# Performance work log

Measured on AMD Instinct MI355X. Metric: run time of the kernel, lower is better.

The kernel has to match this reference:

```python
import jax, jax.numpy as jnp
import numpy as np

# Rates 40MHz -> 60MHz => Fraction(1.5).limit_denominator(1000) = 3/2
UP, DOWN = 3, 2
MAX_RATE = max(UP, DOWN)
HALF_LEN = 10 * MAX_RATE                      # 30 (scipy.resample_poly default)
N_PRE_PAD = DOWN - (HALF_LEN % DOWN)          # 2
N_PRE_REMOVE = (HALF_LEN + N_PRE_PAD) // DOWN # 16
NUMTAPS_LS = 51
TAIL_ZEROS = 100
B, N = 8, 1048576


def _firwin_kaiser(numtaps, cutoff, beta):
    # scipy.signal.firwin(numtaps, cutoff, window=('kaiser', beta)), cutoff in Nyquist units
    m = np.arange(numtaps) - (numtaps - 1) / 2.0
    h = cutoff * np.sinc(cutoff * m)
    h *= np.kaiser(numtaps, beta)
    return h / h.sum()  # unit DC gain


def _band_int(k, f1, f2):
    # integral_{f1}^{f2} cos(pi*k*f) df, elementwise over integer array k
    k = np.asarray(k, dtype=float)
    safe = np.where(k == 0.0, 1.0, np.pi * k)
    return np.where(k == 0.0, f2 - f1, (np.sin(np.pi * k * f2) - np.sin(np.pi * k * f1)) / safe)


def _firls(numtaps, bands, desired):
    # Type-I linear-phase least-squares FIR (constant desired per band, unit weights)
    M = (numtaps - 1) // 2
    k = np.arange(M + 1)
    Q = np.zeros((M + 1, M + 1))
    rhs = np.zeros(M + 1)
    for f1, f2, d in zip(bands[0::2], bands[1::2], desired[0::2]):
        km = k[:, None] - k[None, :]
        kp = k[:, None] + k[None, :]
        Q += 0.5 * (_band_int(km, f1, f2) + _band_int(kp, f1, f2))
        rhs += d * _band_int(k, f1, f2)
    a = np.linalg.solve(Q, rhs)  # A(f) = sum_n a[n] cos(pi n f)
    half = a / 2.0
    half[0] = a[0]
    return np.concatenate([half[:0:-1], half])  # symmetric impulse response


def setup_inputs() -> dict:
    key = jax.random.key(0)
    x = jax.random.normal(key, (B, N), dtype=jnp.float32)
    # resample_poly anti-imaging filter, scaled by UP, with scipy's zero pre-padding
    h = _firwin_kaiser(2 * HALF_LEN + 1, 1.0 / MAX_RATE, 5.0) * UP
    h = np.concatenate([np.zeros(N_PRE_PAD), h])
    cutoff = DOWN / UP
    b = _firls(NUMTAPS_LS, [0.0, cutoff, cutoff + 0.1, 1.0], [1.0, 1.0, 0.0, 0.0])
    return {
        'x': x,
        'h_resample': jnp.asarray(h, jnp.float32),
        'b_fir': jnp.asarray(b, jnp.float32),
    }


def reference(x, h_resample, b_fir):
    b_sz, n = x.shape
    n_in = b_sz * n
    n_out = n_in * UP // DOWN + (1 if (n_in * UP) % DOWN else 0)
    xf = x.reshape(-1)
    Lh = h_resample.shape[0]
    # Fused polyphase resample: full convolution of UP-zero-stuffed signal
    # with h (flipped for true convolution), decimated by DOWN.
    y = jax.lax.conv_general_dilated(
        xf[None, None, :], h_resample[::-1][None, None, :],
        window_strides=(DOWN,), padding=[(Lh - 1, Lh - 1)],
        lhs_dilation=(UP,),
        dimension_numbers=('NCH', 'OIH', 'NCH'))[0, 0]
    u = y[N_PRE_REMOVE:N_PRE_REMOVE + n_out]               # == scipy.resample_poly
    up_padded = jnp.concatenate([u, jnp.zeros((TAIL_ZEROS,), x.dtype)])
    Lb = b_fir.shape[0]
    # lfilter(b, 1, .) == causal FIR: left-pad Lb-1 zeros, same-length output
    filt = jax.lax.conv_general_dilated(
        up_padded[None, None, :], b_fir[::-1][None, None, :],
        window_strides=(1,), padding=[(Lb - 1, 0)],
        dimension_numbers=('NCH', 'OIH', 'NCH'))[0, 0]
    total = n_out + TAIL_ZEROS
    per_b = total // b_sz
    return filt[:b_sz * per_b].reshape(b_sz, per_b)
```

## Files before the change

kernel.cpp:

```cpp
#include <hip/hip_runtime.h>


#define TPB 256
#define RPT 12
#define OTILE (TPB * RPT)
#define XTILE2 2112
#define NTAPS 55
#define CPSTRIDE 56

__global__ void build_coeffs(const float* __restrict__ h,
                             const float* __restrict__ b,
                             float* __restrict__ cp) {
    __shared__ float h_s[63];
    __shared__ float b_s[51];
    const int tid = threadIdx.x;
    if (tid < 63) h_s[tid] = h[tid];
    if (tid < 51) b_s[tid] = b[tid];
    __syncthreads();
    for (int idx = tid; idx < 3 * CPSTRIDE; idx += blockDim.x) {
        const int p = idx / CPSTRIDE;
        const int k = idx - p * CPSTRIDE;
        float acc = 0.0f;
        if (k < NTAPS) {
            const int j = p + 3 * k;
            for (int m = 0; m <= 50; ++m) {
                const int hi = j - 2 * m;
                if (hi >= 0 && hi <= 62) acc += b_s[m] * h_s[hi];
            }
        }
        cp[idx] = acc;
    }
}

__global__ __launch_bounds__(128) void boundary_fix(
    const float* __restrict__ x, const float* __restrict__ h,
    const float* __restrict__ b, float* __restrict__ out,
    int n_in, int n_out, int out_size)
{
    __shared__ float h_s[63];
    __shared__ float b_s[51];
    __shared__ float x_s[64];
    __shared__ float u_s[50];

    const int tid = threadIdx.x;
    if (tid < 63) h_s[tid] = h[tid];
    if (tid < 51) b_s[tid] = b[tid];

    if (blockIdx.x == 0) {
        if (tid < 44) x_s[tid] = (tid < n_in) ? x[tid] : 0.0f;
        __syncthreads();
        if (tid < 50) {
            const int s  = 2 * tid + 32;
            const int p0 = s % 3;
            const int q  = s / 3;
            float u = 0.0f;
            #pragma unroll
            for (int i = 0; i <= 20; ++i) {
                const int xi = q - i;
                u += h_s[p0 + 3 * i] * ((xi >= 0) ? x_s[xi] : 0.0f);
            }
            u_s[tid] = u;
        }
        __syncthreads();
        if (tid < 50) {
            float acc = 0.0f;
            for (int t = 0; t <= tid; ++t) acc += b_s[tid - t] * u_s[t];
            out[tid] = acc;
        }
    } else {
        const int t0   = n_out - 50;
        const int qmin = (2 * t0 + 32) / 3;
        const int xb   = qmin - 20;
        if (tid < 64) {
            const int xi = xb + tid;
            x_s[tid] = (xi >= 0 && xi < n_in) ? x[xi] : 0.0f;
        }
        __syncthreads();
        if (tid < 50) {
            const int t  = t0 + tid;
            const int s  = 2 * t + 32;
            const int p0 = s % 3;
            const int q  = s / 3;
            const int base = q - xb;
            float u = 0.0f;
            #pragma unroll
            for (int i = 0; i <= 20; ++i)
                u += h_s[p0 + 3 * i] * x_s[base - i];
            u_s[tid] = u;
        }
        __syncthreads();
        const int n_tail = out_size - n_out;
        if (tid < n_tail) {
            float acc = 0.0f;
            for (int j = tid; j <= 49; ++j) acc += b_s[tid + 50 - j] * u_s[j];
            out[n_out + tid] = acc;
        }
    }
}

#define GRP12(g, A, B, C, D) {                                          \
    const float4 q2 = c2q[g];                                           \
    const float4 q1 = c1q[g];                                           \
    const float4 q0 = c0q[g];                                           \
                                                               \
    a0  += q2.x * C.z;  a1  += q1.x * C.w;  a2  += q0.x * B.x;          \
    a3  += q2.x * B.x;  a4  += q1.x * B.y;  a5  += q0.x * B.z;          \
    a6  += q2.x * B.z;  a7  += q1.x * B.w;  a8  += q0.x * A.x;          \
    a9  += q2.x * A.x;  a10 += q1.x * A.y;  a11 += q0.x * A.z;          \
                                                               \
    a0  += q2.y * C.y;  a1  += q1.y * C.z;  a2  += q0.y * C.w;          \
    a3  += q2.y * C.w;  a4  += q1.y * B.x;  a5  += q0.y * B.y;          \
    a6  += q2.y * B.y;  a7  += q1.y * B.z;  a8  += q0.y * B.w;          \
    a9  += q2.y * B.w;  a10 += q1.y * A.x;  a11 += q0.y * A.y;          \
                                                               \
    a0  += q2.z * C.x;  a1  += q1.z * C.y;  a2  += q0.z * C.z;          \
    a3  += q2.z * C.z;  a4  += q1.z * C.w;  a5  += q0.z * B.x;          \
    a6  += q2.z * B.x;  a7  += q1.z * B.y;  a8  += q0.z * B.z;          \
    a9  += q2.z * B.z;  a10 += q1.z * B.w;  a11 += q0.z * A.x;          \
                                                               \
    a0  += q2.w * D.w;  a1  += q1.w * C.x;  a2  += q0.w * C.y;          \
    a3  += q2.w * C.y;  a4  += q1.w * C.z;  a5  += q0.w * C.w;          \
    a6  += q2.w * C.w;  a7  += q1.w * B.x;  a8  += q0.w * B.y;          \
    a9  += q2.w * B.y;  a10 += q1.w * B.z;  a11 += q0.w * B.w; }

#define GRP12T(g, A, B, C) {                                            \
    const float4 q2 = c2q[g];                                           \
    const float4 q1 = c1q[g];                                           \
    const float4 q0 = c0q[g];                                           \
    a0  += q2.x * C.z;  a1  += q1.x * C.w;  a2  += q0.x * B.x;          \
    a3  += q2.x * B.x;  a4  += q1.x * B.y;  a5  += q0.x * B.z;          \
    a6  += q2.x * B.z;  a7  += q1.x * B.w;  a8  += q0.x * A.x;          \
    a9  += q2.x * A.x;  a10 += q1.x * A.y;  a11 += q0.x * A.z;          \
    a0  += q2.y * C.y;  a1  += q1.y * C.z;  a2  += q0.y * C.w;          \
    a3  += q2.y * C.w;  a4  += q1.y * B.x;  a5  += q0.y * B.y;          \
    a6  += q2.y * B.y;  a7  += q1.y * B.z;  a8  += q0.y * B.w;          \
    a9  += q2.y * B.w;  a10 += q1.y * A.x;  a11 += q0.y * A.y;          \
    a0  += q2.z * C.x;  a1  += q1.z * C.y;  a2  += q0.z * C.z;          \
    a3  += q2.z * C.z;  a4  += q1.z * C.w;  a5  += q0.z * B.x;          \
    a6  += q2.z * B.x;  a7  += q1.z * B.y;  a8  += q0.z * B.z;          \
    a9  += q2.z * B.z;  a10 += q1.z * B.w;  a11 += q0.z * A.x; }

#define CONV12(SRC) {                                                   \
    const float4 w15 = SRC[15]; const float4 w14 = SRC[14];             \
    const float4 w13 = SRC[13]; const float4 w12 = SRC[12];             \
    const float4 w11 = SRC[11]; const float4 w10 = SRC[10];             \
    const float4 w9  = SRC[9];  const float4 w8  = SRC[8];              \
    const float4 w7  = SRC[7];  const float4 w6  = SRC[6];              \
    const float4 w5  = SRC[5];  const float4 w4  = SRC[4];              \
    const float4 w3  = SRC[3];  const float4 w2  = SRC[2];              \
    const float4 w1  = SRC[1];  const float4 w0  = SRC[0];              \
    __builtin_amdgcn_sched_barrier(0);                                  \
    GRP12( 0, w15, w14, w13, w12);                                      \
    GRP12( 1, w14, w13, w12, w11);                                      \
    GRP12( 2, w13, w12, w11, w10);                                      \
    GRP12( 3, w12, w11, w10, w9);                                       \
    GRP12( 4, w11, w10, w9,  w8);                                       \
    GRP12( 5, w10, w9,  w8,  w7);                                       \
    GRP12( 6, w9,  w8,  w7,  w6);                                       \
    GRP12( 7, w8,  w7,  w6,  w5);                                       \
    GRP12( 8, w7,  w6,  w5,  w4);                                       \
    GRP12( 9, w6,  w5,  w4,  w3);                                       \
    GRP12(10, w5,  w4,  w3,  w2);                                       \
    GRP12(11, w4,  w3,  w2,  w1);                                       \
    GRP12(12, w3,  w2,  w1,  w0);                                       \
    GRP12T(13, w2, w1, w0); }

__global__ __launch_bounds__(TPB) void fused_fast(
    const float* __restrict__ x, const float* __restrict__ cp,
    float* __restrict__ out, int n_in, int n_out)
{
    __shared__ float x_s[XTILE2];

    const int tid = threadIdx.x;
    const int o0  = blockIdx.x * OTILE;
    const int Qb  = (2 * o0 + 30) / 3;
    const int n_tile0 = Qb - 54;

    const float4* c2q = (const float4*)(cp + 2 * CPSTRIDE);
    const float4* c1q = (const float4*)(cp + 1 * CPSTRIDE);
    const float4* c0q = (const float4*)(cp + 0 * CPSTRIDE);

    float a0 = 0.f, a1 = 0.f, a2 = 0.f, a3  = 0.f, a4  = 0.f, a5  = 0.f;
    float a6 = 0.f, a7 = 0.f, a8 = 0.f, a9  = 0.f, a10 = 0.f, a11 = 0.f;

    const bool interior = (n_tile0 >= 0) && (Qb + 2050 <= n_in);
    if (interior) {
        const float4* gx4 = (const float4*)(x + n_tile0 + 8 * tid);
        CONV12(gx4);
    } else {
        for (int i = tid; i < XTILE2; i += TPB) {
            const int n = n_tile0 + i;
            x_s[i] = (n >= 0 && n < n_in) ? x[n] : 0.0f;
        }
        __syncthreads();
        const float4* xs4 = (const float4*)(x_s) + 2 * tid;
        CONV12(xs4);
    }

    const int ob = o0 + RPT * tid;
    if (ob >= 50 && ob + 11 < n_out) {
        float4* o4 = (float4*)(out + ob);
        o4[0] = make_float4(a0, a1, a2,  a3);
        o4[1] = make_float4(a4, a5, a6,  a7);
        o4[2] = make_float4(a8, a9, a10, a11);
    } else {
        const float accs[RPT] = {a0, a1, a2, a3, a4, a5, a6, a7, a8, a9, a10, a11};
#pragma unroll
        for (int d = 0; d < RPT; ++d) {
            const int o = ob + d;
            if (o >= 50 && o < n_out) out[o] = accs[d];
        }
    }
}

extern "C" void kernel_launch(void* const* d_in, const int* in_sizes, int n_in_arrs,
                              void* d_out, int out_size, void* d_ws, size_t ws_size,
                              hipStream_t stream) {
    const float* x = (const float*)d_in[0];
    const float* h = (const float*)d_in[1];
    const float* b = (const float*)d_in[2];
    float* out = (float*)d_out;
    float* cp  = (float*)d_ws;

    const int n_in  = in_sizes[0];
    const int n_out = (int)((long long)n_in * 3 / 2);

    build_coeffs<<<1, 64, 0, stream>>>(h, b, cp);

    const int nblocks = (n_out + OTILE - 1) / OTILE;
    fused_fast<<<nblocks, TPB, 0, stream>>>(x, cp, out, n_in, n_out);
    boundary_fix<<<2, 128, 0, stream>>>(x, h, b, out, n_in, n_out, out_size);
}
```

Before: 119.5 us.

## Make fused kernel persistent over four tiles with register double-buffered prefetch

Each block now handles four consecutive output tiles instead of one, with a fixed grid of 1024 blocks. While computing the current tile from one register set, it loads the next tile's 16 float4 input words into a second set, overlapping global load latency with FMA work. This raises register pressure (two 64-float buffers) and may reduce occupancy. It also hardcodes the grid size and tile count to the test shape.

```diff
diff --git a/kernel.cpp b/kernel.cpp
--- a/kernel.cpp
+++ b/kernel.cpp
@@ -4,6 +4,8 @@
 #define TPB 256
 #define RPT 12
 #define OTILE (TPB * RPT)
+#define TPBK 4
+#define NBLOCKS 1024
 #define XTILE2 2112
 #define NTAPS 55
 #define CPSTRIDE 56
@@ -102,22 +104,18 @@
     const float4 q2 = c2q[g];                                           \
     const float4 q1 = c1q[g];                                           \
     const float4 q0 = c0q[g];                                           \
-                                                               \
     a0  += q2.x * C.z;  a1  += q1.x * C.w;  a2  += q0.x * B.x;          \
     a3  += q2.x * B.x;  a4  += q1.x * B.y;  a5  += q0.x * B.z;          \
     a6  += q2.x * B.z;  a7  += q1.x * B.w;  a8  += q0.x * A.x;          \
     a9  += q2.x * A.x;  a10 += q1.x * A.y;  a11 += q0.x * A.z;          \
-                                                               \
     a0  += q2.y * C.y;  a1  += q1.y * C.z;  a2  += q0.y * C.w;          \
     a3  += q2.y * C.w;  a4  += q1.y * B.x;  a5  += q0.y * B.y;          \
     a6  += q2.y * B.y;  a7  += q1.y * B.z;  a8  += q0.y * B.w;          \
     a9  += q2.y * B.w;  a10 += q1.y * A.x;  a11 += q0.y * A.y;          \
-                                                               \
     a0  += q2.z * C.x;  a1  += q1.z * C.y;  a2  += q0.z * C.z;          \
     a3  += q2.z * C.z;  a4  += q1.z * C.w;  a5  += q0.z * B.x;          \
     a6  += q2.z * B.x;  a7  += q1.z * B.y;  a8  += q0.z * B.z;          \
     a9  += q2.z * B.z;  a10 += q1.z * B.w;  a11 += q0.z * A.x;          \
-                                                               \
     a0  += q2.w * D.w;  a1  += q1.w * C.x;  a2  += q0.w * C.y;          \
     a3  += q2.w * C.y;  a4  += q1.w * C.z;  a5  += q0.w * C.w;          \
     a6  += q2.w * C.w;  a7  += q1.w * B.x;  a8  += q0.w * B.y;          \
@@ -140,30 +138,63 @@
     a6  += q2.z * B.x;  a7  += q1.z * B.y;  a8  += q0.z * B.z;          \
     a9  += q2.z * B.z;  a10 += q1.z * B.w;  a11 += q0.z * A.x; }
 
-#define CONV12(SRC) {                                                   \
-    const float4 w15 = SRC[15]; const float4 w14 = SRC[14];             \
-    const float4 w13 = SRC[13]; const float4 w12 = SRC[12];             \
-    const float4 w11 = SRC[11]; const float4 w10 = SRC[10];             \
-    const float4 w9  = SRC[9];  const float4 w8  = SRC[8];              \
-    const float4 w7  = SRC[7];  const float4 w6  = SRC[6];              \
-    const float4 w5  = SRC[5];  const float4 w4  = SRC[4];              \
-    const float4 w3  = SRC[3];  const float4 w2  = SRC[2];              \
-    const float4 w1  = SRC[1];  const float4 w0  = SRC[0];              \
+#define LOAD16(P, S) {                                                  \
+    P##15 = S[15]; P##14 = S[14]; P##13 = S[13]; P##12 = S[12];         \
+    P##11 = S[11]; P##10 = S[10]; P##9  = S[9];  P##8  = S[8];          \
+    P##7  = S[7];  P##6  = S[6];  P##5  = S[5];  P##4  = S[4];          \
+    P##3  = S[3];  P##2  = S[2];  P##1  = S[1];  P##0  = S[0]; }
+
+#define CONV12R(P) {                                                    \
+    GRP12( 0, P##15, P##14, P##13, P##12);                              \
+    GRP12( 1, P##14, P##13, P##12, P##11);                              \
+    GRP12( 2, P##13, P##12, P##11, P##10);                              \
+    GRP12( 3, P##12, P##11, P##10, P##9);                               \
+    GRP12( 4, P##11, P##10, P##9,  P##8);                               \
+    GRP12( 5, P##10, P##9,  P##8,  P##7);                               \
+    GRP12( 6, P##9,  P##8,  P##7,  P##6);                               \
+    GRP12( 7, P##8,  P##7,  P##6,  P##5);                               \
+    GRP12( 8, P##7,  P##6,  P##5,  P##4);                               \
+    GRP12( 9, P##6,  P##5,  P##4,  P##3);                               \
+    GRP12(10, P##5,  P##4,  P##3,  P##2);                               \
+    GRP12(11, P##4,  P##3,  P##2,  P##1);                               \
+    GRP12(12, P##3,  P##2,  P##1,  P##0);                               \
+    GRP12T(13, P##2, P##1, P##0); }
+
+#define PHASE(CUR, NXT) {                                               \
+    int tnext = tile + 1; if (tnext > tlast) tnext = tlast;             \
+    int nbn = 2048 * tnext - 44;                                        \
+    if (nbn < 0) nbn = 0;                                               \
+    if (nbn > n_in - XTILE2) nbn = n_in - XTILE2;                       \
+    const float4* gn = (const float4*)(x + nbn + 8 * tid);              \
+    LOAD16(NXT, gn);                                                    \
     __builtin_amdgcn_sched_barrier(0);                                  \
-    GRP12( 0, w15, w14, w13, w12);                                      \
-    GRP12( 1, w14, w13, w12, w11);                                      \
-    GRP12( 2, w13, w12, w11, w10);                                      \
-    GRP12( 3, w12, w11, w10, w9);                                       \
-    GRP12( 4, w11, w10, w9,  w8);                                       \
-    GRP12( 5, w10, w9,  w8,  w7);                                       \
-    GRP12( 6, w9,  w8,  w7,  w6);                                       \
-    GRP12( 7, w8,  w7,  w6,  w5);                                       \
-    GRP12( 8, w7,  w6,  w5,  w4);                                       \
-    GRP12( 9, w6,  w5,  w4,  w3);                                       \
-    GRP12(10, w5,  w4,  w3,  w2);                                       \
-    GRP12(11, w4,  w3,  w2,  w1);                                       \
-    GRP12(12, w3,  w2,  w1,  w0);                                       \
-    GRP12T(13, w2, w1, w0); }
+    const int nt0 = 2048 * tile - 44;                                   \
+    if (nt0 < 0 || nt0 + XTILE2 > n_in) {                               \
+        for (int i = tid; i < XTILE2; i += TPB) {                       \
+            const int n = nt0 + i;                                      \
+            x_s[i] = (n >= 0 && n < n_in) ? x[n] : 0.0f;                \
+        }                                                               \
+        __syncthreads();                                                \
+        const float4* xe = (const float4*)(x_s) + 2 * tid;              \
+        LOAD16(CUR, xe);                                                \
+    }                                                                   \
+    float a0=0.f,a1=0.f,a2=0.f,a3=0.f,a4=0.f,a5=0.f;                    \
+    float a6=0.f,a7=0.f,a8=0.f,a9=0.f,a10=0.f,a11=0.f;                  \
+    CONV12R(CUR);                                                       \
+    const int ob = tile * OTILE + 12 * tid;                             \
+    if (ob >= 50 && ob + 11 < n_out) {                                  \
+        float4* o4 = (float4*)(out + ob);                               \
+        o4[0] = make_float4(a0, a1, a2,  a3);                           \
+        o4[1] = make_float4(a4, a5, a6,  a7);                           \
+        o4[2] = make_float4(a8, a9, a10, a11);                          \
+    } else {                                                            \
+        const float accs[RPT] = {a0,a1,a2,a3,a4,a5,a6,a7,a8,a9,a10,a11};\
+        for (int d = 0; d < RPT; ++d) {                                 \
+            const int o = ob + d;                                       \
+            if (o >= 50 && o < n_out) out[o] = accs[d];                 \
+        }                                                               \
+    }                                                                   \
+    tile = tnext; }
 
 __global__ __launch_bounds__(TPB) void fused_fast(
     const float* __restrict__ x, const float* __restrict__ cp,
@@ -171,45 +202,28 @@
 {
     __shared__ float x_s[XTILE2];
 
-    const int tid = threadIdx.x;
-    const int o0  = blockIdx.x * OTILE;
-    const int Qb  = (2 * o0 + 30) / 3;
-    const int n_tile0 = Qb - 54;
+    const int tid   = threadIdx.x;
+    int tile        = blockIdx.x * TPBK;
+    const int tlast = tile + TPBK - 1;
 
     const float4* c2q = (const float4*)(cp + 2 * CPSTRIDE);
     const float4* c1q = (const float4*)(cp + 1 * CPSTRIDE);
     const float4* c0q = (const float4*)(cp + 0 * CPSTRIDE);
 
-    float a0 = 0.f, a1 = 0.f, a2 = 0.f, a3  = 0.f, a4  = 0.f, a5  = 0.f;
-    float a6 = 0.f, a7 = 0.f, a8 = 0.f, a9  = 0.f, a10 = 0.f, a11 = 0.f;
-
-    const bool interior = (n_tile0 >= 0) && (Qb + 2050 <= n_in);
-    if (interior) {
-        const float4* gx4 = (const float4*)(x + n_tile0 + 8 * tid);
-        CONV12(gx4);
-    } else {
-        for (int i = tid; i < XTILE2; i += TPB) {
-            const int n = n_tile0 + i;
-            x_s[i] = (n >= 0 && n < n_in) ? x[n] : 0.0f;
-        }
-        __syncthreads();
-        const float4* xs4 = (const float4*)(x_s) + 2 * tid;
-        CONV12(xs4);
-    }
-
-    const int ob = o0 + RPT * tid;
-    if (ob >= 50 && ob + 11 < n_out) {
-        float4* o4 = (float4*)(out + ob);
-        o4[0] = make_float4(a0, a1, a2,  a3);
-        o4[1] = make_float4(a4, a5, a6,  a7);
-        o4[2] = make_float4(a8, a9, a10, a11);
-    } else {
-        const float accs[RPT] = {a0, a1, a2, a3, a4, a5, a6, a7, a8, a9, a10, a11};
-#pragma unroll
-        for (int d = 0; d < RPT; ++d) {
-            const int o = ob + d;
-            if (o >= 50 && o < n_out) out[o] = accs[d];
-        }
+    float4 A0,A1,A2,A3,A4,A5,A6,A7,A8,A9,A10,A11,A12,A13,A14,A15;
+    float4 B0,B1,B2,B3,B4,B5,B6,B7,B8,B9,B10,B11,B12,B13,B14,B15;
+
+    {
+        int nb0 = 2048 * tile - 44;
+        if (nb0 < 0) nb0 = 0;
+        if (nb0 > n_in - XTILE2) nb0 = n_in - XTILE2;
+        const float4* g0 = (const float4*)(x + nb0 + 8 * tid);
+        LOAD16(A, g0);
+    }
+
+    for (int it = 0; it < TPBK / 2; ++it) {
+        PHASE(A, B);
+        PHASE(B, A);
     }
 }
 
@@ -226,8 +240,6 @@
     const int n_out = (int)((long long)n_in * 3 / 2);
 
     build_coeffs<<<1, 64, 0, stream>>>(h, b, cp);
-
-    const int nblocks = (n_out + OTILE - 1) / OTILE;
-    fused_fast<<<nblocks, TPB, 0, stream>>>(x, cp, out, n_in, n_out);
+    fused_fast<<<NBLOCKS, TPB, 0, stream>>>(x, cp, out, n_in, n_out);
     boundary_fix<<<2, 128, 0, stream>>>(x, h, b, out, n_in, n_out, out_size);
 }
```

New measurement: 127.2 us. 6.4% more time.

## Process four tiles per block with double-buffered async global-to-LDS staging

Applied to the files above, without the earlier changes.

The main kernel now loops over four output tiles per block instead of one, and uses two LDS buffers. While the current tile is being convolved, the next tile's input is prefetched into LDS with global_load_lds async copies. Interior tiles previously read the input straight from global memory into registers; now every tile goes through LDS with a barrier per iteration. The grid size is hard-coded to 1024 blocks, which ties correctness to the fixed problem size, and the async copies are not waited on explicitly before use, so correctness depends on the existing __syncthreads.

```diff
diff --git a/kernel.cpp b/kernel.cpp
--- a/kernel.cpp
+++ b/kernel.cpp
@@ -1,10 +1,14 @@
 #include <hip/hip_runtime.h>
+#include <cstdint>
 
 
 #define TPB 256
 #define RPT 12
 #define OTILE (TPB * RPT)
-#define XTILE2 2112
+#define NTILES 4096
+#define TPBK 4
+#define NBLOCKS (NTILES / TPBK)
+#define XT 2112
 #define NTAPS 55
 #define CPSTRIDE 56
 
@@ -98,26 +102,42 @@
     }
 }
 
+__device__ __forceinline__ void async_copy16(const float* gp, float* lp) {
+    auto g = (const __attribute__((address_space(1))) unsigned int*)(uintptr_t)gp;
+    auto l = (__attribute__((address_space(3))) unsigned int*)(uintptr_t)lp;
+    __builtin_amdgcn_global_load_lds(g, l, 16, 0, 0);
+}
+
+__device__ __forceinline__ void stage_dma(const float* __restrict__ x,
+                                          float* dst, int base, int tid) {
+    async_copy16(x + base + 4 * tid,        dst + 4 * tid);
+    async_copy16(x + base + 1024 + 4 * tid, dst + 1024 + 4 * tid);
+}
+
+__device__ __forceinline__ void stage_edge(const float* __restrict__ x,
+                                           float* dst, int base, int n_in, int tid) {
+    for (int i = tid; i < XT; i += TPB) {
+        const int n = base + i;
+        dst[i] = (n >= 0 && n < n_in) ? x[n] : 0.0f;
+    }
+}
+
 #define GRP12(g, A, B, C, D) {                                          \
     const float4 q2 = c2q[g];                                           \
     const float4 q1 = c1q[g];                                           \
     const float4 q0 = c0q[g];                                           \
-                                                               \
     a0  += q2.x * C.z;  a1  += q1.x * C.w;  a2  += q0.x * B.x;          \
     a3  += q2.x * B.x;  a4  += q1.x * B.y;  a5  += q0.x * B.z;          \
     a6  += q2.x * B.z;  a7  += q1.x * B.w;  a8  += q0.x * A.x;          \
     a9  += q2.x * A.x;  a10 += q1.x * A.y;  a11 += q0.x * A.z;          \
-                                                               \
     a0  += q2.y * C.y;  a1  += q1.y * C.z;  a2  += q0.y * C.w;          \
     a3  += q2.y * C.w;  a4  += q1.y * B.x;  a5  += q0.y * B.y;          \
     a6  += q2.y * B.y;  a7  += q1.y * B.z;  a8  += q0.y * B.w;          \
     a9  += q2.y * B.w;  a10 += q1.y * A.x;  a11 += q0.y * A.y;          \
-                                                               \
     a0  += q2.z * C.x;  a1  += q1.z * C.y;  a2  += q0.z * C.z;          \
     a3  += q2.z * C.z;  a4  += q1.z * C.w;  a5  += q0.z * B.x;          \
     a6  += q2.z * B.x;  a7  += q1.z * B.y;  a8  += q0.z * B.z;          \
     a9  += q2.z * B.z;  a10 += q1.z * B.w;  a11 += q0.z * A.x;          \
-                                                               \
     a0  += q2.w * D.w;  a1  += q1.w * C.x;  a2  += q0.w * C.y;          \
     a3  += q2.w * C.y;  a4  += q1.w * C.z;  a5  += q0.w * C.w;          \
     a6  += q2.w * C.w;  a7  += q1.w * B.x;  a8  += q0.w * B.y;          \
@@ -140,76 +160,91 @@
     a6  += q2.z * B.x;  a7  += q1.z * B.y;  a8  += q0.z * B.z;          \
     a9  += q2.z * B.z;  a10 += q1.z * B.w;  a11 += q0.z * A.x; }
 
-#define CONV12(SRC) {                                                   \
-    const float4 w15 = SRC[15]; const float4 w14 = SRC[14];             \
-    const float4 w13 = SRC[13]; const float4 w12 = SRC[12];             \
-    const float4 w11 = SRC[11]; const float4 w10 = SRC[10];             \
-    const float4 w9  = SRC[9];  const float4 w8  = SRC[8];              \
-    const float4 w7  = SRC[7];  const float4 w6  = SRC[6];              \
-    const float4 w5  = SRC[5];  const float4 w4  = SRC[4];              \
-    const float4 w3  = SRC[3];  const float4 w2  = SRC[2];              \
-    const float4 w1  = SRC[1];  const float4 w0  = SRC[0];              \
-    __builtin_amdgcn_sched_barrier(0);                                  \
-    GRP12( 0, w15, w14, w13, w12);                                      \
-    GRP12( 1, w14, w13, w12, w11);                                      \
-    GRP12( 2, w13, w12, w11, w10);                                      \
-    GRP12( 3, w12, w11, w10, w9);                                       \
-    GRP12( 4, w11, w10, w9,  w8);                                       \
-    GRP12( 5, w10, w9,  w8,  w7);                                       \
-    GRP12( 6, w9,  w8,  w7,  w6);                                       \
-    GRP12( 7, w8,  w7,  w6,  w5);                                       \
-    GRP12( 8, w7,  w6,  w5,  w4);                                       \
-    GRP12( 9, w6,  w5,  w4,  w3);                                       \
-    GRP12(10, w5,  w4,  w3,  w2);                                       \
-    GRP12(11, w4,  w3,  w2,  w1);                                       \
-    GRP12(12, w3,  w2,  w1,  w0);                                       \
-    GRP12T(13, w2, w1, w0); }
+#define CONV12R(P) {                                                    \
+    GRP12( 0, P##15, P##14, P##13, P##12);                              \
+    GRP12( 1, P##14, P##13, P##12, P##11);                              \
+    GRP12( 2, P##13, P##12, P##11, P##10);                              \
+    GRP12( 3, P##12, P##11, P##10, P##9);                               \
+    GRP12( 4, P##11, P##10, P##9,  P##8);                               \
+    GRP12( 5, P##10, P##9,  P##8,  P##7);                               \
+    GRP12( 6, P##9,  P##8,  P##7,  P##6);                               \
+    GRP12( 7, P##8,  P##7,  P##6,  P##5);                               \
+    GRP12( 8, P##7,  P##6,  P##5,  P##4);                               \
+    GRP12( 9, P##6,  P##5,  P##4,  P##3);                               \
+    GRP12(10, P##5,  P##4,  P##3,  P##2);                               \
+    GRP12(11, P##4,  P##3,  P##2,  P##1);                               \
+    GRP12(12, P##3,  P##2,  P##1,  P##0);                               \
+    GRP12T(13, P##2, P##1, P##0); }
 
 __global__ __launch_bounds__(TPB) void fused_fast(
     const float* __restrict__ x, const float* __restrict__ cp,
     float* __restrict__ out, int n_in, int n_out)
 {
-    __shared__ float x_s[XTILE2];
+    __shared__ alignas(16) float xs0[XT];
+    __shared__ alignas(16) float xs1[XT];
 
     const int tid = threadIdx.x;
-    const int o0  = blockIdx.x * OTILE;
-    const int Qb  = (2 * o0 + 30) / 3;
-    const int n_tile0 = Qb - 54;
+    const int t0  = blockIdx.x * TPBK;
 
     const float4* c2q = (const float4*)(cp + 2 * CPSTRIDE);
     const float4* c1q = (const float4*)(cp + 1 * CPSTRIDE);
     const float4* c0q = (const float4*)(cp + 0 * CPSTRIDE);
 
-    float a0 = 0.f, a1 = 0.f, a2 = 0.f, a3  = 0.f, a4  = 0.f, a5  = 0.f;
-    float a6 = 0.f, a7 = 0.f, a8 = 0.f, a9  = 0.f, a10 = 0.f, a11 = 0.f;
-
-    const bool interior = (n_tile0 >= 0) && (Qb + 2050 <= n_in);
-    if (interior) {
-        const float4* gx4 = (const float4*)(x + n_tile0 + 8 * tid);
-        CONV12(gx4);
-    } else {
-        for (int i = tid; i < XTILE2; i += TPB) {
-            const int n = n_tile0 + i;
-            x_s[i] = (n >= 0 && n < n_in) ? x[n] : 0.0f;
-        }
-        __syncthreads();
-        const float4* xs4 = (const float4*)(x_s) + 2 * tid;
-        CONV12(xs4);
-    }
-
-    const int ob = o0 + RPT * tid;
-    if (ob >= 50 && ob + 11 < n_out) {
-        float4* o4 = (float4*)(out + ob);
-        o4[0] = make_float4(a0, a1, a2,  a3);
-        o4[1] = make_float4(a4, a5, a6,  a7);
-        o4[2] = make_float4(a8, a9, a10, a11);
-    } else {
-        const float accs[RPT] = {a0, a1, a2, a3, a4, a5, a6, a7, a8, a9, a10, a11};
-#pragma unroll
-        for (int d = 0; d < RPT; ++d) {
-            const int o = ob + d;
-            if (o >= 50 && o < n_out) out[o] = accs[d];
-        }
+    {
+        const int base = 2048 * t0 - 44;
+        if (base >= 0 && base + 2104 <= n_in) {
+            stage_dma(x, xs0, base, tid);
+            if (tid < 56) xs0[2048 + tid] = x[base + 2048 + tid];
+        } else {
+            stage_edge(x, xs0, base, n_in, tid);
+        }
+    }
+    __syncthreads();
+
+    for (int k = 0; k < TPBK; ++k) {
+        const int tile = t0 + k;
+        float* cur = (k & 1) ? xs1 : xs0;
+        float* nxt = (k & 1) ? xs0 : xs1;
+
+        const int nbase = 2048 * (tile + 1) - 44;
+        const bool havenext = (k + 1 < TPBK);
+        const bool nxt_int  = (nbase >= 0) && (nbase + 2104 <= n_in);
+        if (havenext) {
+            if (nxt_int) stage_dma(x, nxt, nbase, tid);
+            else         stage_edge(x, nxt, nbase, n_in, tid);
+        }
+        __builtin_amdgcn_sched_barrier(0);
+
+        const float4* s4 = (const float4*)cur + 2 * tid;
+        const float4 W15 = s4[15], W14 = s4[14], W13 = s4[13], W12 = s4[12];
+        const float4 W11 = s4[11], W10 = s4[10], W9  = s4[9],  W8  = s4[8];
+        const float4 W7  = s4[7],  W6  = s4[6],  W5  = s4[5],  W4  = s4[4];
+        const float4 W3  = s4[3],  W2  = s4[2],  W1  = s4[1],  W0  = s4[0];
+        __builtin_amdgcn_sched_barrier(0);
+
+        float a0 = 0.f, a1 = 0.f, a2 = 0.f, a3  = 0.f, a4  = 0.f, a5  = 0.f;
+        float a6 = 0.f, a7 = 0.f, a8 = 0.f, a9  = 0.f, a10 = 0.f, a11 = 0.f;
+        CONV12R(W);
+        __builtin_amdgcn_sched_barrier(0);
+
+        if (havenext && nxt_int) {
+            if (tid < 56) nxt[2048 + tid] = x[nbase + 2048 + tid];
+        }
+
+        const int ob = tile * OTILE + RPT * tid;
+        if (ob >= 50 && ob + 11 < n_out) {
+            float4* o4 = (float4*)(out + ob);
+            o4[0] = make_float4(a0, a1, a2,  a3);
+            o4[1] = make_float4(a4, a5, a6,  a7);
+            o4[2] = make_float4(a8, a9, a10, a11);
+        } else {
+            const float accs[RPT] = {a0,a1,a2,a3,a4,a5,a6,a7,a8,a9,a10,a11};
+            for (int d = 0; d < RPT; ++d) {
+                const int o = ob + d;
+                if (o >= 50 && o < n_out) out[o] = accs[d];
+            }
+        }
+        __syncthreads();
     }
 }
 
@@ -226,8 +261,6 @@
     const int n_out = (int)((long long)n_in * 3 / 2);
 
     build_coeffs<<<1, 64, 0, stream>>>(h, b, cp);
-
-    const int nblocks = (n_out + OTILE - 1) / OTILE;
-    fused_fast<<<nblocks, TPB, 0, stream>>>(x, cp, out, n_in, n_out);
+    fused_fast<<<NBLOCKS, TPB, 0, stream>>>(x, cp, out, n_in, n_out);
     boundary_fix<<<2, 128, 0, stream>>>(x, h, b, out, n_in, n_out, out_size);
 }
```

Measured after the change: 143.8 us. +20.4%, slower.
